# Kernel optimization log

Measured on AMD Instinct MI355X. Metric: run time of the kernel, lower is better.

The kernel has to match this reference:

```python
import jax, jax.numpy as jnp
import numpy as np

N_NODES, N_EDGES, F_DIM, H_DIM = 50000, 800000, 128, 128
BN_EPS = 1e-3  # keras BatchNormalization default epsilon


def setup_inputs() -> dict:
    key = jax.random.key(0)
    k0, k1, k2 = jax.random.split(key, 3)
    edge_pairs = jax.random.randint(k0, (N_EDGES, 2), 0, N_NODES, dtype=jnp.int64 if jax.config.jax_enable_x64 else jnp.int32)
    node_features = jax.random.normal(k1, (N_NODES, F_DIM), dtype=jnp.float32)
    W = jax.random.normal(k2, (F_DIM, H_DIM), dtype=jnp.float32) * (1.0 / np.sqrt(F_DIM))
    b = jnp.zeros((H_DIM,), jnp.float32)
    gamma = jnp.ones((H_DIM,), jnp.float32)
    beta = jnp.zeros((H_DIM,), jnp.float32)
    moving_mean = jnp.zeros((H_DIM,), jnp.float32)
    moving_var = jnp.ones((H_DIM,), jnp.float32)
    return {"edge_pairs": edge_pairs, "node_features": node_features, "W": W, "b": b,
            "gamma": gamma, "beta": beta, "moving_mean": moving_mean, "moving_var": moving_var}


def reference(edge_pairs, node_features, W, b, gamma, beta, moving_mean, moving_var):
    src = edge_pairs[:, 0]
    dst = edge_pairs[:, 1]
    n = node_features.shape[0]

    # linear transform (dropout inactive: training=False)
    t = node_features @ W + b  # [N, H]

    # out-degree by source node
    deg = jax.ops.segment_sum(jnp.ones(src.shape[0], t.dtype), src, num_segments=n)  # [N]
    inv_sqrt_deg = jnp.power(deg, -0.5)  # matches tf.pow(d, -0.5)

    # degree-normalized neighbour messages: d_src^-1/2 * d_dst^-1/2 * t[dst]
    scale = (inv_sqrt_deg[src] * inv_sqrt_deg[dst])[:, None]  # [E,1]
    nb_sum = jax.ops.segment_sum(t[dst] * scale, src, num_segments=n)  # [N, H]

    # source term: segment_mean(deg[src] * t[src]) ; empty segments -> 0 (tf semantics)
    msg = deg[src][:, None] * t[src]  # [E, H]
    seg = jax.ops.segment_sum(msg, src, num_segments=n)  # [N, H]
    src_mean = jnp.where(deg[:, None] > 0, seg / jnp.maximum(deg, 1.0)[:, None], 0.0)

    agg = 0.5 * nb_sum + 0.5 * src_mean

    # batchnorm, inference mode (moving statistics)
    return (agg - moving_mean) * jax.lax.rsqrt(moving_var + BN_EPS) * gamma + beta
```

## Files before the change

### kernel.cpp

```cpp
#include <hip/hip_runtime.h>
#include <math.h>

#define BN_EPS 0.001f
#define CHUNK 2048
#define MAXBUCK 1024

typedef __attribute__((ext_vector_type(8))) short bf16x8;
typedef __attribute__((ext_vector_type(4))) float f32x4;
typedef __attribute__((ext_vector_type(2))) float f32x2;

__device__ inline unsigned bf16rne(float f) {
  unsigned u = __float_as_uint(f);
  return (u + 0x7fffu + ((u >> 16) & 1u)) >> 16;
}
__device__ inline float bflo(unsigned r) { return __uint_as_float(r << 16); }
__device__ inline float bfhi(unsigned r) { return __uint_as_float(r & 0xffff0000u); }

__global__ __launch_bounds__(256) void k_ehist(const int2* __restrict__ ep, int ne,
                                               int nbuck, int* __restrict__ ghist) {
  __shared__ int h[MAXBUCK];
  int c = blockIdx.x, t = threadIdx.x;
  for (int i = t; i < nbuck; i += 256) h[i] = 0;
  __syncthreads();
  int base = c * CHUNK;
  int end = min(base + CHUNK, ne);
  for (int e = base + t; e < end; e += 256) atomicAdd(&h[ep[e].x >> 6], 1);
  __syncthreads();
  int* row = ghist + (size_t)c * nbuck;
  for (int i = t; i < nbuck; i += 256) row[i] = h[i];
}

__global__ __launch_bounds__(512) void k_bscan(int* __restrict__ ghist, int nchunk,
                                               int nbuck, int* __restrict__ btot) {
  __shared__ int s0[512], s1[512];
  int b = blockIdx.x, t = threadIdx.x;
  int v = (t < nchunk) ? ghist[(size_t)t * nbuck + b] : 0;
  s0[t] = v;
  __syncthreads();
  int* src = s0; int* dst = s1;
  for (int off = 1; off < 512; off <<= 1) {
    int x = src[t];
    if (t >= off) x += src[t - off];
    dst[t] = x;
    __syncthreads();
    int* tmp = src; src = dst; dst = tmp;
  }
  if (t < nchunk) ghist[(size_t)t * nbuck + b] = src[t] - v;
  if (t == 0) btot[b] = src[511];
}

__global__ __launch_bounds__(1024) void k_bbase(const int* __restrict__ btot, int nbuck,
                                                int* __restrict__ bbase) {
  __shared__ int s0[1024], s1[1024];
  int t = threadIdx.x;
  int v = (t < nbuck) ? btot[t] : 0;
  s0[t] = v;
  __syncthreads();
  int* src = s0; int* dst = s1;
  for (int off = 1; off < 1024; off <<= 1) {
    int x = src[t];
    if (t >= off) x += src[t - off];
    dst[t] = x;
    __syncthreads();
    int* tmp = src; src = dst; dst = tmp;
  }
  if (t < nbuck) bbase[t] = src[t] - v;
}

__global__ __launch_bounds__(256) void k_ebin(const int2* __restrict__ ep, int ne,
                                              int nbuck, const int* __restrict__ ghist,
                                              const int* __restrict__ bbase,
                                              unsigned* __restrict__ bins) {
  __shared__ int cur[MAXBUCK];
  int c = blockIdx.x, t = threadIdx.x;
  const int* row = ghist + (size_t)c * nbuck;
  for (int i = t; i < nbuck; i += 256) cur[i] = bbase[i] + row[i];
  __syncthreads();
  int base = c * CHUNK;
  int end = min(base + CHUNK, ne);
  for (int e = base + t; e < end; e += 256) {
    int2 p = ep[e];
    int pos = atomicAdd(&cur[p.x >> 6], 1);
    bins[pos] = (unsigned)p.y | ((unsigned)(p.x & 63) << 17);
  }
}

__global__ __launch_bounds__(256) void k_bfinal(const int* __restrict__ bbase,
                                                const int* __restrict__ btot,
                                                const unsigned* __restrict__ bins,
                                                int n, int* __restrict__ deg,
                                                float* __restrict__ isd,
                                                int* __restrict__ offsets,
                                                int* __restrict__ csr_dst) {
  __shared__ int h[64];
  __shared__ int cur[64];
  int bk = blockIdx.x, t = threadIdx.x;
  if (t < 64) h[t] = 0;
  __syncthreads();
  int s = bbase[bk], cnt = btot[bk];
  for (int i = t; i < cnt; i += 256) atomicAdd(&h[bins[s + i] >> 17], 1);
  __syncthreads();
  if (t == 0) {
    int run = s;
    for (int j = 0; j < 64; ++j) { cur[j] = run; run += h[j]; }
  }
  __syncthreads();
  if (t < 64) {
    int node = (bk << 6) + t;
    if (node < n) {
      deg[node] = h[t];
      offsets[node] = cur[t];
      isd[node] = 1.0f / sqrtf((float)h[t]);
    }
  }
  __syncthreads();
  for (int i = t; i < cnt; i += 256) {
    unsigned r = bins[s + i];
    int pos = atomicAdd(&cur[r >> 17], 1);
    csr_dst[pos] = (int)(r & 0x1FFFFu);
  }
}

__global__ __launch_bounds__(1024, 4) void k_gemm(const float* __restrict__ X,
                                                  const float* __restrict__ W,
                                                  const float* __restrict__ b,
                                                  const float* __restrict__ isd,
                                                  const int* __restrict__ deg,
                                                  unsigned* __restrict__ Th,
                                                  unsigned char* __restrict__ Tb8, int M) {
  __shared__ unsigned short WhL[16384];
  __shared__ unsigned short WlL[16384];
  int tid = threadIdx.x;

#pragma unroll
  for (int it = 0; it < 4; ++it) {
    int q = tid + it * 1024;
    int k = q >> 5;
    int c0 = (q & 31) * 4;
    float4 v = ((const float4*)W)[q];
    float vv[4] = {v.x, v.y, v.z, v.w};
#pragma unroll
    for (int j2 = 0; j2 < 4; ++j2) {
      int col = c0 + j2;
      float x = vv[j2];
      unsigned short hh = (unsigned short)(__float_as_uint(x) >> 16);
      float rem = x - __uint_as_float((unsigned)hh << 16);
      int frag = ((col >> 4) << 2) | (k >> 5);
      int ln = (((k >> 3) & 3) << 4) | (col & 15);
      int addr = frag * 512 + ln * 8 + (k & 7);
      WhL[addr] = hh;
      WlL[addr] = (unsigned short)bf16rne(rem);
    }
  }

  int wave = tid >> 6, lane = tid & 63;
  int r16 = lane & 15, kq = lane >> 4;
  int rowbase = blockIdx.x * 256 + wave * 16;
  int arow = rowbase + r16;
  bool aok = arow < M;
  const float* xr = X + ((size_t)arow << 7);

  bf16x8 ah[4], al[4];
#pragma unroll
  for (int ks = 0; ks < 4; ++ks) {
    int k0 = ks * 32 + kq * 8;
    float4 v0 = aok ? *(const float4*)(xr + k0) : make_float4(0.f, 0.f, 0.f, 0.f);
    float4 v1 = aok ? *(const float4*)(xr + k0 + 4) : make_float4(0.f, 0.f, 0.f, 0.f);
    float f[8] = {v0.x, v0.y, v0.z, v0.w, v1.x, v1.y, v1.z, v1.w};
    bf16x8 h8, l8;
#pragma unroll
    for (int j = 0; j < 8; ++j) {
      unsigned short hh = (unsigned short)(__float_as_uint(f[j]) >> 16);
      float rem = f[j] - __uint_as_float((unsigned)hh << 16);
      h8[j] = (short)hh;
      l8[j] = (short)bf16rne(rem);
    }
    ah[ks] = h8;
    al[ks] = l8;
  }
  __syncthreads();

  f32x4 acc[8] = {};
#pragma unroll
  for (int ct = 0; ct < 8; ++ct) {
#pragma unroll
    for (int ks = 0; ks < 4; ++ks) {
      int base = (ct * 4 + ks) * 512 + lane * 8;
      bf16x8 bh = *(const bf16x8*)&WhL[base];
      bf16x8 bl = *(const bf16x8*)&WlL[base];
      acc[ct] = __builtin_amdgcn_mfma_f32_16x16x32_bf16(ah[ks], bh, acc[ct], 0, 0, 0);
      acc[ct] = __builtin_amdgcn_mfma_f32_16x16x32_bf16(ah[ks], bl, acc[ct], 0, 0, 0);
      acc[ct] = __builtin_amdgcn_mfma_f32_16x16x32_bf16(al[ks], bh, acc[ct], 0, 0, 0);
    }
  }

  int orow[4];
  float isdr[4], degr[4];
#pragma unroll
  for (int r = 0; r < 4; ++r) {
    orow[r] = rowbase + kq * 4 + r;
    bool ok = orow[r] < M;
    isdr[r] = ok ? isd[orow[r]] : 0.f;
    degr[r] = ok ? 0.5f * (float)deg[orow[r]] : 0.f;
  }
#pragma unroll
  for (int ct = 0; ct < 8; ++ct) {
    int col = ct * 16 + r16;
    float bias = b[col];
#pragma unroll
    for (int r = 0; r < 4; ++r) {
      float v = acc[ct][r] + bias;
      bool ok = orow[r] < M;
      float sv = v * isdr[r];
      float so = __shfl_xor(sv, 1);
      int pk01 = __builtin_amdgcn_cvt_pk_fp8_f32(sv, so, 0, false);
      int pk23 = __shfl_xor(pk01, 2);
      if (ok && (r16 & 3) == 0) {
        unsigned dword = ((unsigned)pk01 & 0xFFFFu) | ((unsigned)pk23 << 16);
        *(unsigned*)&Tb8[((size_t)orow[r] << 7) + ct * 16 + r16] = dword;
      }
      float tv = degr[r] * v;
      float to = __shfl_xor(tv, 1);
      if (ok && !(r16 & 1)) {
        unsigned pk = bf16rne(tv) | (bf16rne(to) << 16);
        Th[((size_t)orow[r] << 6) + ct * 8 + (r16 >> 1)] = pk;
      }
    }
  }
}

__global__ __launch_bounds__(256) void k_gather(
    const unsigned* __restrict__ Th, const unsigned char* __restrict__ Tb8,
    const int* __restrict__ deg, const float* __restrict__ isd,
    const int* __restrict__ offsets, const int* __restrict__ csr_dst,
    const float* __restrict__ mm, const float* __restrict__ var,
    const float* __restrict__ gamma, const float* __restrict__ beta,
    float* __restrict__ out, int n) {
  int wave = threadIdx.x >> 6;
  int lane = threadIdx.x & 63;
  int half = lane >> 5;
  int l32 = lane & 31;
  int pair = blockIdx.x * 4 + wave;
  int i = 2 * pair + half;
  if (2 * pair >= n) return;
  bool iok = i < n;
  int degi = iok ? deg[i] : 0;
  int start = iok ? offsets[i] : 0;
  int dother = __shfl(degi, lane ^ 32);
  int dmax = max(degi, dother);
  const unsigned* myrows = (const unsigned*)Tb8 + l32;

  f32x2 accA[8] = {}, accB[8] = {};
  int sl = l32 & 7;
  int dv = (sl < degi) ? csr_dst[start + sl] : i;
  for (int e = 0; e < dmax; e += 8) {
    int dv_next = (e + 8 + sl < degi) ? csr_dst[start + e + 8 + sl] : i;
    unsigned r8[8];
#pragma unroll
    for (int j = 0; j < 8; ++j) {
      int idx = __shfl(dv, (half << 5) + j);
      r8[j] = myrows[(unsigned)idx << 5];
    }
#pragma unroll
    for (int j = 0; j < 8; ++j) {
      int rr = (e + j < degi) ? (int)r8[j] : 0;
      accA[j] += __builtin_amdgcn_cvt_pk_f32_fp8(rr, false);
      accB[j] += __builtin_amdgcn_cvt_pk_f32_fp8(rr, true);
    }
    dv = dv_next;
  }
  f32x2 sA = ((accA[0] + accA[1]) + (accA[2] + accA[3])) +
             ((accA[4] + accA[5]) + (accA[6] + accA[7]));
  f32x2 sB = ((accB[0] + accB[1]) + (accB[2] + accB[3])) +
             ((accB[4] + accB[5]) + (accB[6] + accB[7]));

  if (!iok) return;
  float4 aggv = make_float4(0.f, 0.f, 0.f, 0.f);
  if (degi > 0) {
    uint2 th = ((const uint2*)(Th + ((size_t)i << 6)))[l32];
    float hsi = 0.5f * isd[i];
    aggv.x = hsi * sA.x + bflo(th.x);
    aggv.y = hsi * sA.y + bfhi(th.x);
    aggv.z = hsi * sB.x + bflo(th.y);
    aggv.w = hsi * sB.y + bfhi(th.y);
  }
  float4 mmv = ((const float4*)mm)[l32];
  float4 vv = ((const float4*)var)[l32];
  float4 gv = ((const float4*)gamma)[l32];
  float4 bv = ((const float4*)beta)[l32];
  float4 res;
  res.x = (aggv.x - mmv.x) * rsqrtf(vv.x + BN_EPS) * gv.x + bv.x;
  res.y = (aggv.y - mmv.y) * rsqrtf(vv.y + BN_EPS) * gv.y + bv.y;
  res.z = (aggv.z - mmv.z) * rsqrtf(vv.z + BN_EPS) * gv.z + bv.z;
  res.w = (aggv.w - mmv.w) * rsqrtf(vv.w + BN_EPS) * gv.w + bv.w;
  ((float4*)(out + ((size_t)i << 7)))[l32] = res;
}

static inline size_t align_up(size_t x) { return (x + 255) & ~(size_t)255; }

extern "C" void kernel_launch(void* const* d_in, const int* in_sizes, int n_in,
                              void* d_out, int out_size, void* d_ws, size_t ws_size,
                              hipStream_t stream) {
  const int2* ep = (const int2*)d_in[0];
  const float* X = (const float*)d_in[1];
  const float* W = (const float*)d_in[2];
  const float* b = (const float*)d_in[3];
  const float* gamma = (const float*)d_in[4];
  const float* beta = (const float*)d_in[5];
  const float* mm = (const float*)d_in[6];
  const float* var = (const float*)d_in[7];
  float* out = (float*)d_out;

  const int ne = in_sizes[0] / 2;
  const int n = in_sizes[1] / 128;
  const int nbuck = (n + 63) >> 6;
  const int nchunk = (ne + CHUNK - 1) / CHUNK;

  char* p = (char*)d_ws;
  int* deg = (int*)p;        p += align_up((size_t)n * 4);
  float* isd = (float*)p;    p += align_up((size_t)n * 4);
  int* offsets = (int*)p;    p += align_up((size_t)n * 4);
  int* btot = (int*)p;       p += align_up((size_t)nbuck * 4);
  int* bbase = (int*)p;      p += align_up((size_t)nbuck * 4);
  int* ghist = (int*)p;      p += align_up((size_t)nchunk * nbuck * 4);
  int* csr_dst = (int*)p;    p += align_up((size_t)ne * 4);
  unsigned* bins = (unsigned*)p; p += align_up((size_t)ne * 4);
  unsigned* Th = (unsigned*)p;   p += align_up((size_t)n * 64 * 4);
  unsigned char* Tb8 = (unsigned char*)p; p += align_up((size_t)n * 128);

  k_ehist<<<nchunk, 256, 0, stream>>>(ep, ne, nbuck, ghist);
  k_bscan<<<nbuck, 512, 0, stream>>>(ghist, nchunk, nbuck, btot);
  k_bbase<<<1, 1024, 0, stream>>>(btot, nbuck, bbase);
  k_ebin<<<nchunk, 256, 0, stream>>>(ep, ne, nbuck, ghist, bbase, bins);
  k_bfinal<<<nbuck, 256, 0, stream>>>(bbase, btot, bins, n, deg, isd, offsets, csr_dst);
  k_gemm<<<(n + 255) / 256, 1024, 0, stream>>>(X, W, b, isd, deg, Th, Tb8, n);
  int pairs = (n + 1) / 2;
  k_gather<<<(pairs + 3) / 4, 256, 0, stream>>>(Th, Tb8, deg, isd, offsets, csr_dst,
                                                mm, var, gamma, beta, out, n);
}
```

Measured before the change: 80.79 us.

## Sort nodes by degree within each bucket to balance gather half-waves

Within each 64-node bucket, k_bfinal now runs an odd-even transposition sort by degree and writes a node permutation. The gather kernel processes nodes in that order, so the two nodes sharing a wave have similar degrees. This cuts the divergence where a wave loops to the larger of its two degrees. In exchange it adds 64 sync phases per bucket block, an extra indirection load, and a less coalesced output write order.

```diff
diff --git a/kernel.cpp b/kernel.cpp
--- a/kernel.cpp
+++ b/kernel.cpp
@@ -91,9 +91,12 @@
                                                 int n, int* __restrict__ deg,
                                                 float* __restrict__ isd,
                                                 int* __restrict__ offsets,
-                                                int* __restrict__ csr_dst) {
+                                                int* __restrict__ csr_dst,
+                                                int* __restrict__ order) {
   __shared__ int h[64];
   __shared__ int cur[64];
+  __shared__ int skey[64];
+  __shared__ int sval[64];
   int bk = blockIdx.x, t = threadIdx.x;
   if (t < 64) h[t] = 0;
   __syncthreads();
@@ -107,13 +110,31 @@
   __syncthreads();
   if (t < 64) {
     int node = (bk << 6) + t;
-    if (node < n) {
+    bool ok = node < n;
+    if (ok) {
       deg[node] = h[t];
       offsets[node] = cur[t];
       isd[node] = 1.0f / sqrtf((float)h[t]);
     }
-  }
-  __syncthreads();
+    skey[t] = ok ? h[t] : 0x7FFFFFFF;
+    sval[t] = ok ? node : 0x7FFFFFFF;
+  }
+  __syncthreads();
+  for (int ph = 0; ph < 64; ++ph) {
+    if (t < 32) {
+      int idx = 2 * t + (ph & 1);
+      if (idx + 1 < 64) {
+        int k0 = skey[idx], k1 = skey[idx + 1];
+        if (k0 > k1) {
+          int v0 = sval[idx], v1 = sval[idx + 1];
+          skey[idx] = k1; skey[idx + 1] = k0;
+          sval[idx] = v1; sval[idx + 1] = v0;
+        }
+      }
+    }
+    __syncthreads();
+  }
+  if (t < 64) order[(bk << 6) + t] = sval[t];
   for (int i = t; i < cnt; i += 256) {
     unsigned r = bins[s + i];
     int pos = atomicAdd(&cur[r >> 17], 1);
@@ -233,6 +254,7 @@
     const unsigned* __restrict__ Th, const unsigned char* __restrict__ Tb8,
     const int* __restrict__ deg, const float* __restrict__ isd,
     const int* __restrict__ offsets, const int* __restrict__ csr_dst,
+    const int* __restrict__ order, int nent,
     const float* __restrict__ mm, const float* __restrict__ var,
     const float* __restrict__ gamma, const float* __restrict__ beta,
     float* __restrict__ out, int n) {
@@ -241,9 +263,11 @@
   int half = lane >> 5;
   int l32 = lane & 31;
   int pair = blockIdx.x * 4 + wave;
-  int i = 2 * pair + half;
-  if (2 * pair >= n) return;
-  bool iok = i < n;
+  int ent = 2 * pair + half;
+  if (2 * pair >= nent) return;
+  int i = (ent < nent) ? order[ent] : 0x7FFFFFFF;
+  bool iok = (unsigned)i < (unsigned)n;
+  int irow = iok ? i : 0;
   int degi = iok ? deg[i] : 0;
   int start = iok ? offsets[i] : 0;
   int dother = __shfl(degi, lane ^ 32);
@@ -252,9 +276,9 @@
 
   f32x2 accA[8] = {}, accB[8] = {};
   int sl = l32 & 7;
-  int dv = (sl < degi) ? csr_dst[start + sl] : i;
+  int dv = (sl < degi) ? csr_dst[start + sl] : irow;
   for (int e = 0; e < dmax; e += 8) {
-    int dv_next = (e + 8 + sl < degi) ? csr_dst[start + e + 8 + sl] : i;
+    int dv_next = (e + 8 + sl < degi) ? csr_dst[start + e + 8 + sl] : irow;
     unsigned r8[8];
 #pragma unroll
     for (int j = 0; j < 8; ++j) {
@@ -322,6 +346,7 @@
   int* offsets = (int*)p;    p += align_up((size_t)n * 4);
   int* btot = (int*)p;       p += align_up((size_t)nbuck * 4);
   int* bbase = (int*)p;      p += align_up((size_t)nbuck * 4);
+  int* order = (int*)p;      p += align_up((size_t)nbuck * 64 * 4);
   int* ghist = (int*)p;      p += align_up((size_t)nchunk * nbuck * 4);
   int* csr_dst = (int*)p;    p += align_up((size_t)ne * 4);
   unsigned* bins = (unsigned*)p; p += align_up((size_t)ne * 4);
@@ -332,9 +357,12 @@
   k_bscan<<<nbuck, 512, 0, stream>>>(ghist, nchunk, nbuck, btot);
   k_bbase<<<1, 1024, 0, stream>>>(btot, nbuck, bbase);
   k_ebin<<<nchunk, 256, 0, stream>>>(ep, ne, nbuck, ghist, bbase, bins);
-  k_bfinal<<<nbuck, 256, 0, stream>>>(bbase, btot, bins, n, deg, isd, offsets, csr_dst);
+  k_bfinal<<<nbuck, 256, 0, stream>>>(bbase, btot, bins, n, deg, isd, offsets,
+                                      csr_dst, order);
   k_gemm<<<(n + 255) / 256, 1024, 0, stream>>>(X, W, b, isd, deg, Th, Tb8, n);
-  int pairs = (n + 1) / 2;
+  int nent = nbuck * 64;
+  int pairs = nent / 2;
   k_gather<<<(pairs + 3) / 4, 256, 0, stream>>>(Th, Tb8, deg, isd, offsets, csr_dst,
-                                                mm, var, gamma, beta, out, n);
-}
+                                                order, nent, mm, var, gamma, beta,
+                                                out, n);
+}
```

After: 89.68 us. +11.0%, slower.
